# Kernel tuning notes

Hardware: AMD Instinct MI355X
Metric: run time of the kernel (lower is better)

## Reference

```python
import jax, jax.numpy as jnp
import numpy as np
import math

BS, S, D, H, DFF, L = 32, 512, 512, 8, 2048, 2
DK = D // H
K_INDEX = 5
NEG = -1e32


def _xavier(key, shape):
    fan_out, fan_in = shape[-2], shape[-1]
    lim = math.sqrt(6.0 / (fan_in + fan_out))
    return jax.random.uniform(key, shape, minval=-lim, maxval=lim, dtype=jnp.float32)


def _cosine_pe():
    pos = np.arange(S, dtype=np.float32)[:, None]
    div = np.exp(np.arange(0, D, 2, dtype=np.float32) * -(math.log(10000.0) / D))
    pe = np.zeros((S, D), dtype=np.float32)
    pe[:, 0::2] = np.sin(pos * div)
    pe[:, 1::2] = np.cos(pos * div)
    return jnp.asarray(pe)[None]  # [1,S,D]


def setup_inputs() -> dict:
    key = jax.random.key(0)
    ks = jax.random.split(key, 8)
    return {
        'q_embed_data': jax.random.normal(ks[0], (BS, S, D), jnp.float32),
        'qa_embed_data': jax.random.normal(ks[1], (BS, S, D), jnp.float32),
        'pe': _cosine_pe(),
        'Wk': _xavier(ks[2], (L, D, D)), 'bk': jnp.zeros((L, D)),
        'Wv': _xavier(ks[3], (L, D, D)), 'bv': jnp.zeros((L, D)),
        'Wo': _xavier(ks[4], (L, D, D)), 'bo': jnp.zeros((L, D)),
        'W1': _xavier(ks[5], (L, DFF, D)), 'b1': jnp.zeros((L, DFF)),
        'W2': _xavier(ks[6], (L, D, DFF)), 'b2': jnp.zeros((L, D)),
        'ln1w': jnp.ones((L, D)), 'ln1b': jnp.zeros((L, D)),
        'ln2w': jnp.ones((L, D)), 'ln2b': jnp.zeros((L, D)),
    }


def _ln(x, w, b):
    m = jnp.mean(x, axis=-1, keepdims=True)
    v = jnp.mean((x - m) ** 2, axis=-1, keepdims=True)
    return (x - m) / jnp.sqrt(v + 1e-5) * w + b


def _forward(q_embed_data, qa_embed_data, pe, Wk, bk, Wv, bv, Wo, bo,
             W1, b1, W2, b2, ln1w, ln1b, ln2w, ln2b):
    x = q_embed_data + pe[:, :S]
    y = qa_embed_data + pe[:, :S]
    # src_mask = (triu(ones, k=0) == 0): only strictly-lower positions allowed (row 0 fully masked)
    causal = jnp.tril(jnp.ones((S, S), bool), k=-1)
    attn_weights = None
    for l in range(L):
        # kq_same: q uses k_linear
        q = (x @ Wk[l].T + bk[l]).reshape(BS, S, H, DK).transpose(0, 2, 1, 3)
        k = q  # identical projection of identical input (key=query=x)
        v = (y @ Wv[l].T + bv[l]).reshape(BS, S, H, DK).transpose(0, 2, 1, 3)
        scores = jnp.einsum('bhqd,bhkd->bhqk', q, k) / math.sqrt(DK)
        scores = jnp.where(causal, scores, NEG)
        scores = jax.nn.softmax(scores, axis=-1)
        # sparseattn: for rows >= K_INDEX keep only entries >= k-th largest, re-softmax
        sb = scores[:, :, K_INDEX:, :]
        thr = jax.lax.top_k(sb, K_INDEX)[0][..., -1:]  # k-th largest per row
        sb = jnp.where(sb - thr >= 0, sb, NEG)
        scores = jnp.concatenate([scores[:, :, :K_INDEX, :], sb], axis=2)
        scores = jax.nn.softmax(scores, axis=-1)
        attn_weights = scores  # before_dropout_scores (before zero_pad)
        scores = scores.at[:, :, 0, :].set(0.0)  # zero_pad row 0
        out = jnp.einsum('bhqk,bhkd->bhqd', scores, v)
        out = out.transpose(0, 2, 1, 3).reshape(BS, S, D) @ Wo[l].T + bo[l]
        x = _ln(x + out, ln1w[l], ln1b[l])
        ff = jax.nn.relu(x @ W1[l].T + b1[l]) @ W2[l].T + b2[l]
        x = _ln(x + ff, ln2w[l], ln2b[l])
    return x, attn_weights


def reference(q_embed_data, qa_embed_data, pe, Wk, bk, Wv, bv, Wo, bo,
              W1, b1, W2, b2, ln1w, ln1b, ln2w, ln2b):
    return _forward(q_embed_data, qa_embed_data, pe, Wk, bk, Wv, bv, Wo, bo,
                    W1, b1, W2, b2, ln1w, ln1b, ln2w, ln2b)
```

## Files before the change

kernel.cpp:

```cpp
#include <hip/hip_runtime.h>
#include <hip/hip_bf16.h>
#include <math.h>

#define BSZ 32
#define SEQ 512
#define DIM 512
#define NH 8
#define DKH 64
#define DFFN 2048
#define NL 2
#define KIDX 5
#define NEGV -1e32f

typedef float f32x4 __attribute__((ext_vector_type(4)));
typedef short bf16x8 __attribute__((ext_vector_type(8)));
typedef unsigned short ushort_t;
typedef __attribute__((address_space(1))) void gvoid;
typedef __attribute__((address_space(3))) void lvoid;

__device__ __forceinline__ void gload_lds16(const void* g, void* l) {
    __builtin_amdgcn_global_load_lds((gvoid*)(uintptr_t)g, (lvoid*)l, 16, 0, 0);
}

__device__ __forceinline__ float wmaxf(float v) {
    #pragma unroll
    for (int m = 32; m > 0; m >>= 1) v = fmaxf(v, __shfl_xor(v, m));
    return v;
}
__device__ __forceinline__ float wsumf(float v) {
    #pragma unroll
    for (int m = 32; m > 0; m >>= 1) v += __shfl_xor(v, m);
    return v;
}
__device__ __forceinline__ int wsumi(int v) {
    #pragma unroll
    for (int m = 32; m > 0; m >>= 1) v += __shfl_xor(v, m);
    return v;
}

__device__ __forceinline__ unsigned int bf16_rne(float x) {
    unsigned int u = __float_as_uint(x);
    return (u + 0x7fffu + ((u >> 16) & 1u)) >> 16;
}
__device__ __forceinline__ void split3_8(const float* xs, unsigned int* hh,
                                         unsigned int* hm, unsigned int* hl) {
    #pragma unroll
    for (int e = 0; e < 8; e++) {
        float x = xs[e];
        unsigned int h0 = bf16_rne(x);
        float r1 = x - __uint_as_float(h0 << 16);
        unsigned int h1 = bf16_rne(r1);
        float r2 = r1 - __uint_as_float(h1 << 16);
        hh[e] = h0; hm[e] = h1; hl[e] = bf16_rne(r2);
    }
}
__device__ __forceinline__ uint4 pack8(const unsigned int* h) {
    return make_uint4(h[0] | (h[1] << 16), h[2] | (h[3] << 16),
                      h[4] | (h[5] << 16), h[6] | (h[7] << 16));
}

__device__ __forceinline__ f32x4 mfma_bf16(bf16x8 a, bf16x8 b, f32x4 c) {
    return __builtin_amdgcn_mfma_f32_16x16x32_bf16(a, b, c, 0, 0, 0);
}

__global__ void add_pe_new(const float* __restrict__ q, const float* __restrict__ qa,
                           const float* __restrict__ pe, float* __restrict__ x,
                           ushort_t* __restrict__ ypl, size_t yelems, int n8) {
    int i = blockIdx.x * 256 + threadIdx.x;
    if (i >= n8) return;
    size_t base = (size_t)i * 8;
    size_t pb = base & (size_t)(SEQ * DIM - 1);
    float4 a0 = *(const float4*)(q + base), a1 = *(const float4*)(q + base + 4);
    float4 b0 = *(const float4*)(qa + base), b1 = *(const float4*)(qa + base + 4);
    float4 p0 = *(const float4*)(pe + pb), p1 = *(const float4*)(pe + pb + 4);
    float4 x0 = make_float4(a0.x + p0.x, a0.y + p0.y, a0.z + p0.z, a0.w + p0.w);
    float4 x1 = make_float4(a1.x + p1.x, a1.y + p1.y, a1.z + p1.z, a1.w + p1.w);
    *(float4*)(x + base) = x0;
    *(float4*)(x + base + 4) = x1;
    float ys[8] = {b0.x + p0.x, b0.y + p0.y, b0.z + p0.z, b0.w + p0.w,
                   b1.x + p1.x, b1.y + p1.y, b1.z + p1.z, b1.w + p1.w};
    unsigned int hh[8], hm[8], hl[8];
    split3_8(ys, hh, hm, hl);
    *(uint4*)(ypl + base) = pack8(hh);
    *(uint4*)(ypl + yelems + base) = pack8(hm);
    *(uint4*)(ypl + 2 * yelems + base) = pack8(hl);
}

__global__ void split3w(const float* __restrict__ W, ushort_t* __restrict__ out,
                        size_t elems, int n8) {
    int i = blockIdx.x * 256 + threadIdx.x;
    if (i >= n8) return;
    size_t base = (size_t)i * 8;
    float4 a0 = *(const float4*)(W + base), a1 = *(const float4*)(W + base + 4);
    float xs[8] = {a0.x, a0.y, a0.z, a0.w, a1.x, a1.y, a1.z, a1.w};
    unsigned int hh[8], hm[8], hl[8];
    split3_8(xs, hh, hm, hl);
    *(uint4*)(out + base) = pack8(hh);
    *(uint4*)(out + elems + base) = pack8(hm);
    *(uint4*)(out + 2 * elems + base) = pack8(hl);
}

template <int RELU>
__global__ __launch_bounds__(256)
void gemm_bt(const float* __restrict__ A, const float* __restrict__ B,
             const float* __restrict__ bias, float* __restrict__ C,
             int M, int N, int K) {
    __shared__ float As[32][132];
    __shared__ float Bs[32][132];
    const int tid = threadIdx.x;
    const int tx = tid & 15, ty = tid >> 4;
    const int m0 = blockIdx.y * 128, n0 = blockIdx.x * 128;
    float acc[8][8] = {};
    for (int k0 = 0; k0 < K; k0 += 32) {
        #pragma unroll
        for (int s = tid; s < 1024; s += 256) {
            int r = (s & 15) | ((s >> 7) << 4);
            int c4 = (s >> 4) & 7;
            float4 va = *(const float4*)(A + (size_t)(m0 + r) * K + k0 + c4 * 4);
            As[c4 * 4 + 0][r] = va.x; As[c4 * 4 + 1][r] = va.y;
            As[c4 * 4 + 2][r] = va.z; As[c4 * 4 + 3][r] = va.w;
            float4 vb = *(const float4*)(B + (size_t)(n0 + r) * K + k0 + c4 * 4);
            Bs[c4 * 4 + 0][r] = vb.x; Bs[c4 * 4 + 1][r] = vb.y;
            Bs[c4 * 4 + 2][r] = vb.z; Bs[c4 * 4 + 3][r] = vb.w;
        }
        __syncthreads();
        #pragma unroll 8
        for (int kk = 0; kk < 32; kk++) {
            float a[8], b[8];
            *(float4*)&a[0] = *(const float4*)&As[kk][ty * 8];
            *(float4*)&a[4] = *(const float4*)&As[kk][ty * 8 + 4];
            *(float4*)&b[0] = *(const float4*)&Bs[kk][tx * 8];
            *(float4*)&b[4] = *(const float4*)&Bs[kk][tx * 8 + 4];
            #pragma unroll
            for (int i = 0; i < 8; i++)
                #pragma unroll
                for (int j = 0; j < 8; j++)
                    acc[i][j] = fmaf(a[i], b[j], acc[i][j]);
        }
        __syncthreads();
    }
    float bv[8];
    *(float4*)&bv[0] = *(const float4*)(bias + n0 + tx * 8);
    *(float4*)&bv[4] = *(const float4*)(bias + n0 + tx * 8 + 4);
    #pragma unroll
    for (int i = 0; i < 8; i++) {
        float out[8];
        #pragma unroll
        for (int j = 0; j < 8; j++) {
            float v = acc[i][j] + bv[j];
            if (RELU) v = fmaxf(v, 0.f);
            out[j] = v;
        }
        float* cp = C + (size_t)(m0 + ty * 8 + i) * N + n0 + tx * 8;
        *(float4*)cp = *(float4*)&out[0];
        *(float4*)(cp + 4) = *(float4*)&out[4];
    }
}

__global__ __launch_bounds__(256)
void scores128_kernel(const float* __restrict__ q, float* __restrict__ pbuf) {
    const int bh = blockIdx.y, b = bh >> 3, h = bh & 7;
    const int x = blockIdx.x;
    const int it = (x >= 6) ? 3 : (x >= 3) ? 2 : (x >= 1) ? 1 : 0;
    const int jt = x - it * (it + 1) / 2;
    const int m0 = it * 128, n0 = jt * 128;
    __shared__ float Qi[64][132];
    __shared__ float Qj[64][132];
    const float* qbase = q + (size_t)b * SEQ * DIM + h * DKH;
    const int tid = threadIdx.x;
    for (int s = tid; s < 2048; s += 256) {
        int row = (s & 15) | ((s >> 8) << 4);
        int c4 = (s >> 4) & 15;
        float4 vi = *(const float4*)(qbase + (size_t)(m0 + row) * DIM + c4 * 4);
        Qi[c4 * 4 + 0][row] = vi.x; Qi[c4 * 4 + 1][row] = vi.y;
        Qi[c4 * 4 + 2][row] = vi.z; Qi[c4 * 4 + 3][row] = vi.w;
        float4 vj = *(const float4*)(qbase + (size_t)(n0 + row) * DIM + c4 * 4);
        Qj[c4 * 4 + 0][row] = vj.x; Qj[c4 * 4 + 1][row] = vj.y;
        Qj[c4 * 4 + 2][row] = vj.z; Qj[c4 * 4 + 3][row] = vj.w;
    }
    __syncthreads();
    const int tx = tid & 15, ty = tid >> 4;
    float acc[8][8] = {};
    #pragma unroll 4
    for (int d = 0; d < 64; d++) {
        float a[8], bb[8];
        *(float4*)&a[0] = *(const float4*)&Qi[d][ty * 8];
        *(float4*)&a[4] = *(const float4*)&Qi[d][ty * 8 + 4];
        *(float4*)&bb[0] = *(const float4*)&Qj[d][tx * 8];
        *(float4*)&bb[4] = *(const float4*)&Qj[d][tx * 8 + 4];
        #pragma unroll
        for (int i = 0; i < 8; i++)
            #pragma unroll
            for (int j = 0; j < 8; j++)
                acc[i][j] = fmaf(a[i], bb[j], acc[i][j]);
    }
    float* prow = pbuf + ((size_t)bh * SEQ + m0) * SEQ + n0;
    #pragma unroll
    for (int i = 0; i < 8; i++) {
        int gi = m0 + ty * 8 + i;
        #pragma unroll
        for (int jq = 0; jq < 2; jq++) {
            float o[4];
            #pragma unroll
            for (int j = 0; j < 4; j++) {
                int gj = n0 + tx * 8 + jq * 4 + j;
                o[j] = (gj < gi) ? acc[i][jq * 4 + j] * 0.125f : NEGV;
            }
            *(float4*)(prow + (size_t)(ty * 8 + i) * SEQ + tx * 8 + jq * 4) = *(float4*)o;
        }
    }
}

template <int RELU, int OUTP, int NP>
__global__ __launch_bounds__(256) void gemm3p(
    const ushort_t* __restrict__ Apl, size_t Aelems, int lda,
    const ushort_t* __restrict__ Bpl, size_t Belems, int ldb,
    const float* __restrict__ bias,
    float* __restrict__ C, ushort_t* __restrict__ Cpl, size_t Celems,
    int ldc, int K) {
    constexpr int BB = NP * 512;
    __shared__ uint4 lds[2 * NP * 512];
    const int tid = threadIdx.x, lane = tid & 63, wid = tid >> 6;
    const int wm = wid >> 1, wn = wid & 1;
    const int m0 = blockIdx.y * 128, n0 = blockIdx.x * 128;
    const int lrow = lane & 15, lkof = (lane >> 4) * 8;
    f32x4 acc[4][4] = {};
    for (int k0 = 0; k0 < K; k0 += 32) {
        #pragma unroll
        for (int t = 0; t < 4 * NP; t++) {
            int cc = wid + t * 4;
            bool isB = cc >= 8 * NP;
            int c2 = isB ? (cc - 8 * NP) : cc;
            int p = c2 >> 3, fi = c2 & 7;
            const ushort_t* pb = isB ? (Bpl + (size_t)p * Belems) : (Apl + (size_t)p * Aelems);
            int ld = isB ? ldb : lda;
            int r0 = isB ? n0 : m0;
            const ushort_t* src = pb + (size_t)(r0 + fi * 16 + lrow) * ld + k0 + lkof;
            gload_lds16(src, &lds[(isB ? BB : 0) + p * 512 + fi * 64]);
        }
        __syncthreads();
        const bf16x8* ldsb = (const bf16x8*)lds;
        bf16x8 afr[4][NP];
        #pragma unroll
        for (int fm = 0; fm < 4; fm++)
            #pragma unroll
            for (int p = 0; p < NP; p++)
                afr[fm][p] = ldsb[p * 512 + (wm * 4 + fm) * 64 + lane];
        #pragma unroll
        for (int fn = 0; fn < 4; fn++) {
            bf16x8 b0 = ldsb[BB + 0 * 512 + (wn * 4 + fn) * 64 + lane];
            bf16x8 b1 = ldsb[BB + 1 * 512 + (wn * 4 + fn) * 64 + lane];
            bf16x8 b2;
            if constexpr (NP == 3) b2 = ldsb[BB + 2 * 512 + (wn * 4 + fn) * 64 + lane];
            #pragma unroll
            for (int fm = 0; fm < 4; fm++) {
                f32x4 t = acc[fm][fn];
                if constexpr (NP == 3) {
                    t = mfma_bf16(afr[fm][0], b0, t);
                    t = mfma_bf16(afr[fm][1], b0, t);
                    t = mfma_bf16(afr[fm][2], b0, t);
                    t = mfma_bf16(afr[fm][0], b1, t);
                    t = mfma_bf16(afr[fm][1], b1, t);
                    t = mfma_bf16(afr[fm][0], b2, t);
                } else {
                    t = mfma_bf16(afr[fm][0], b0, t);
                    t = mfma_bf16(afr[fm][1], b0, t);
                    t = mfma_bf16(afr[fm][0], b1, t);
                }
                acc[fm][fn] = t;
            }
        }
        __syncthreads();
    }
    #pragma unroll
    for (int fm = 0; fm < 4; fm++) {
        int row0 = m0 + (wm * 4 + fm) * 16 + (lane >> 4) * 4;
        #pragma unroll
        for (int fn = 0; fn < 4; fn++) {
            int col = n0 + (wn * 4 + fn) * 16 + (lane & 15);
            float bv = bias[col];
            f32x4 a = acc[fm][fn];
            #pragma unroll
            for (int r = 0; r < 4; r++) {
                int row = row0 + r;
                float val = a[r] + bv;
                if (RELU) val = fmaxf(val, 0.f);
                if constexpr (OUTP == 0) {
                    C[(size_t)row * ldc + col] = val;
                } else {
                    unsigned int h0 = bf16_rne(val);
                    float r1 = val - __uint_as_float(h0 << 16);
                    unsigned int h1 = bf16_rne(r1);
                    size_t o = (size_t)row * ldc + col;
                    Cpl[o] = (ushort_t)h0;
                    Cpl[Celems + o] = (ushort_t)h1;
                    if constexpr (NP == 3) {
                        float r2 = r1 - __uint_as_float(h1 << 16);
                        Cpl[2 * Celems + o] = (ushort_t)bf16_rne(r2);
                    }
                }
            }
        }
    }
}

template <int NP>
__global__ __launch_bounds__(256) void mm6av_pl(const float* __restrict__ pbuf,
                                                const float* __restrict__ vt,
                                                ushort_t* __restrict__ Opl, size_t Oelems) {
    constexpr int BBASE = NP * 512;
    __shared__ uint4 lds[NP * 512 + NP * 256];
    const int tid = threadIdx.x, lane = tid & 63, wid = tid >> 6;
    const int bh = blockIdx.y, b = bh >> 3, h = bh & 7, rb = blockIdx.x;
    const int m0 = rb * 128;
    const float* A = pbuf + (size_t)bh * SEQ * SEQ;
    const float* B = vt + (size_t)bh * DKH * SEQ;
    const int kmax = rb ? (rb + 1) * 128 : SEQ;

    f32x4 acc[2][4] = {};
    for (int k0 = 0; k0 < kmax; k0 += 32) {
        for (int c = tid; c < 12 * 64; c += 256) {
            int fi = c >> 6, lc = c & 63;
            const float* src = (fi < 8)
                ? A + (size_t)(m0 + fi * 16 + (lc & 15)) * SEQ + k0 + (lc >> 4) * 8
                : B + (size_t)((fi - 8) * 16 + (lc & 15)) * SEQ + k0 + (lc >> 4) * 8;
            float4 x0 = *(const float4*)src;
            float4 x1 = *(const float4*)(src + 4);
            float xs[8] = {x0.x, x0.y, x0.z, x0.w, x1.x, x1.y, x1.z, x1.w};
            unsigned int hh[8], hm[8], hl[8];
            split3_8(xs, hh, hm, hl);
            int base, fstride;
            if (fi < 8) { base = fi * 64 + lc; fstride = 512; }
            else { base = BBASE + (fi - 8) * 64 + lc; fstride = 256; }
            lds[base] = pack8(hh);
            lds[base + fstride] = pack8(hm);
            if (NP == 3) lds[base + 2 * fstride] = pack8(hl);
        }
        __syncthreads();
        const bf16x8* ldsb = (const bf16x8*)lds;
        bf16x8 afr[2][NP];
        #pragma unroll
        for (int fm = 0; fm < 2; fm++)
            #pragma unroll
            for (int p = 0; p < NP; p++)
                afr[fm][p] = ldsb[p * 512 + (wid * 2 + fm) * 64 + lane];
        #pragma unroll
        for (int fn = 0; fn < 4; fn++) {
            bf16x8 b0 = ldsb[BBASE + 0 * 256 + fn * 64 + lane];
            bf16x8 b1 = ldsb[BBASE + 1 * 256 + fn * 64 + lane];
            bf16x8 b2;
            if constexpr (NP == 3) b2 = ldsb[BBASE + 2 * 256 + fn * 64 + lane];
            #pragma unroll
            for (int fm = 0; fm < 2; fm++) {
                f32x4 t = acc[fm][fn];
                if constexpr (NP == 3) {
                    t = mfma_bf16(afr[fm][0], b0, t);
                    t = mfma_bf16(afr[fm][1], b0, t);
                    t = mfma_bf16(afr[fm][2], b0, t);
                    t = mfma_bf16(afr[fm][0], b1, t);
                    t = mfma_bf16(afr[fm][1], b1, t);
                    t = mfma_bf16(afr[fm][0], b2, t);
                } else {
                    t = mfma_bf16(afr[fm][0], b0, t);
                    t = mfma_bf16(afr[fm][1], b0, t);
                    t = mfma_bf16(afr[fm][0], b1, t);
                }
                acc[fm][fn] = t;
            }
        }
        __syncthreads();
    }
    #pragma unroll
    for (int fm = 0; fm < 2; fm++) {
        int row0 = m0 + (wid * 2 + fm) * 16 + (lane >> 4) * 4;
        #pragma unroll
        for (int fn = 0; fn < 4; fn++) {
            int col = fn * 16 + (lane & 15);
            f32x4 a = acc[fm][fn];
            #pragma unroll
            for (int r = 0; r < 4; r++) {
                int row = row0 + r;
                float val = (row == 0) ? 0.f : a[r];
                unsigned int h0 = bf16_rne(val);
                float r1 = val - __uint_as_float(h0 << 16);
                unsigned int h1 = bf16_rne(r1);
                size_t o = ((size_t)b * SEQ + row) * DIM + h * DKH + col;
                Opl[o] = (ushort_t)h0;
                Opl[Oelems + o] = (ushort_t)h1;
                if constexpr (NP == 3) {
                    float r2 = r1 - __uint_as_float(h1 << 16);
                    Opl[2 * Oelems + o] = (ushort_t)bf16_rne(r2);
                }
            }
        }
    }
}

__global__ __launch_bounds__(256) void transpose_v_kernel(const float* __restrict__ v,
                                                          float* __restrict__ vt) {
    const int bh = blockIdx.y, jt = blockIdx.x;
    const int b = bh >> 3, h = bh & 7;
    __shared__ float L[64][65];
    const int tid = threadIdx.x;
    for (int s = tid; s < 1024; s += 256) {
        int jj = s >> 4, d4 = s & 15;
        float4 x = *(const float4*)(v + ((size_t)(b * SEQ) + jt * 64 + jj) * DIM + h * DKH + d4 * 4);
        L[jj][d4 * 4 + 0] = x.x; L[jj][d4 * 4 + 1] = x.y;
        L[jj][d4 * 4 + 2] = x.z; L[jj][d4 * 4 + 3] = x.w;
    }
    __syncthreads();
    int d = tid >> 2, jq = tid & 3;
    float* dst = vt + ((size_t)bh * DKH + d) * SEQ + jt * 64 + jq * 16;
    #pragma unroll
    for (int c4 = 0; c4 < 4; c4++) {
        float4 o = make_float4(L[jq * 16 + c4 * 4 + 0][d], L[jq * 16 + c4 * 4 + 1][d],
                               L[jq * 16 + c4 * 4 + 2][d], L[jq * 16 + c4 * 4 + 3][d]);
        *(float4*)(dst + c4 * 4) = o;
    }
}

__global__ __launch_bounds__(256)
void softmax_topk_kernel(float* __restrict__ pbuf) {
    const int wid = threadIdx.x >> 6, lane = threadIdx.x & 63;
    const int i = blockIdx.x * 4 + wid;
    const size_t row = (size_t)blockIdx.y * SEQ + i;
    float* p = pbuf + row * SEQ;
    float v[8];
    {
        int j0 = lane * 4;
        if (j0 < i) {
            float4 x0 = *(const float4*)(p + j0);
            v[0] = (j0 + 0 < i) ? x0.x : NEGV;
            v[1] = (j0 + 1 < i) ? x0.y : NEGV;
            v[2] = (j0 + 2 < i) ? x0.z : NEGV;
            v[3] = (j0 + 3 < i) ? x0.w : NEGV;
        } else { v[0] = v[1] = v[2] = v[3] = NEGV; }
        int j1 = 256 + j0;
        if (j1 < i) {
            float4 x1 = *(const float4*)(p + j1);
            v[4] = (j1 + 0 < i) ? x1.x : NEGV;
            v[5] = (j1 + 1 < i) ? x1.y : NEGV;
            v[6] = (j1 + 2 < i) ? x1.z : NEGV;
            v[7] = (j1 + 3 < i) ? x1.w : NEGV;
        } else { v[4] = v[5] = v[6] = v[7] = NEGV; }
    }
    float lm = v[0];
    #pragma unroll
    for (int e = 1; e < 8; e++) lm = fmaxf(lm, v[e]);
    float m1 = wmaxf(lm);
    float ls = 0.f;
    #pragma unroll
    for (int e = 0; e < 8; e++) { v[e] = expf(v[e] - m1); ls += v[e]; }
    float Z = wsumf(ls);
    #pragma unroll
    for (int e = 0; e < 8; e++) v[e] = v[e] / Z;
    float thr = -INFINITY;
    if (i >= KIDX) {
        int remaining = KIDX;
        float cut = INFINITY;
        #pragma unroll 1
        for (int iter = 0; iter < KIDX; iter++) {
            float l2 = -INFINITY;
            #pragma unroll
            for (int e = 0; e < 8; e++) if (v[e] < cut) l2 = fmaxf(l2, v[e]);
            float m2 = wmaxf(l2);
            int lc = 0;
            #pragma unroll
            for (int e = 0; e < 8; e++) if (v[e] == m2) lc++;
            int c = wsumi(lc);
            if (c >= remaining) { thr = m2; break; }
            remaining -= c; cut = m2;
        }
    }
    float lpm = v[0];
    #pragma unroll
    for (int e = 1; e < 8; e++) lpm = fmaxf(lpm, v[e]);
    float pm = wmaxf(lpm);
    float t[8];
    float ls2 = 0.f;
    #pragma unroll
    for (int e = 0; e < 8; e++) {
        bool keep = (i >= KIDX) ? (v[e] >= thr) : true;
        t[e] = keep ? expf(v[e] - pm) : 0.f;
        ls2 += t[e];
    }
    float Z2 = wsumf(ls2);
    #pragma unroll
    for (int e = 0; e < 8; e++) t[e] = t[e] / Z2;
    *(float4*)(p + lane * 4) = make_float4(t[0], t[1], t[2], t[3]);
    *(float4*)(p + 256 + lane * 4) = make_float4(t[4], t[5], t[6], t[7]);
}

template <int EMIT>
__global__ __launch_bounds__(64)
void add_ln_kernel(const float* __restrict__ x, const float* __restrict__ t,
                   const float* __restrict__ w, const float* __restrict__ b,
                   float* __restrict__ dst, ushort_t* __restrict__ dpl, size_t delems) {
    const size_t row = blockIdx.x;
    const int lane = threadIdx.x;
    const float* xr = x + row * DIM;
    const float* tr = t + row * DIM;
    float v[8];
    {
        float4 a0 = *(const float4*)(xr + lane * 4);
        float4 t0 = *(const float4*)(tr + lane * 4);
        float4 a1 = *(const float4*)(xr + 256 + lane * 4);
        float4 t1 = *(const float4*)(tr + 256 + lane * 4);
        v[0] = a0.x + t0.x; v[1] = a0.y + t0.y; v[2] = a0.z + t0.z; v[3] = a0.w + t0.w;
        v[4] = a1.x + t1.x; v[5] = a1.y + t1.y; v[6] = a1.z + t1.z; v[7] = a1.w + t1.w;
    }
    float ls = 0.f;
    #pragma unroll
    for (int e = 0; e < 8; e++) ls += v[e];
    float mean = wsumf(ls) / (float)DIM;
    float ld = 0.f;
    #pragma unroll
    for (int e = 0; e < 8; e++) { float d = v[e] - mean; ld += d * d; }
    float var = wsumf(ld) / (float)DIM;
    float den = sqrtf(var + 1e-5f);
    float wv[8], bv[8];
    *(float4*)&wv[0] = *(const float4*)(w + lane * 4);
    *(float4*)&wv[4] = *(const float4*)(w + 256 + lane * 4);
    *(float4*)&bv[0] = *(const float4*)(b + lane * 4);
    *(float4*)&bv[4] = *(const float4*)(b + 256 + lane * 4);
    float o[8];
    #pragma unroll
    for (int e = 0; e < 8; e++) o[e] = (v[e] - mean) / den * wv[e] + bv[e];
    float* dr = dst + row * DIM;
    *(float4*)(dr + lane * 4) = make_float4(o[0], o[1], o[2], o[3]);
    *(float4*)(dr + 256 + lane * 4) = make_float4(o[4], o[5], o[6], o[7]);
    if constexpr (EMIT) {
        unsigned int hh[8], hm[8], hl[8];
        split3_8(o, hh, hm, hl);
        size_t base0 = row * DIM + lane * 4;
        size_t base1 = base0 + 256;
        #pragma unroll
        for (int p = 0; p < 3; p++) {
            const unsigned int* hp = (p == 0) ? hh : (p == 1) ? hm : hl;
            *(uint2*)(dpl + p * delems + base0) =
                make_uint2(hp[0] | (hp[1] << 16), hp[2] | (hp[3] << 16));
            *(uint2*)(dpl + p * delems + base1) =
                make_uint2(hp[4] | (hp[5] << 16), hp[6] | (hp[7] << 16));
        }
    }
}

extern "C" void kernel_launch(void* const* d_in, const int* in_sizes, int n_in,
                              void* d_out, int out_size, void* d_ws, size_t ws_size,
                              hipStream_t stream) {
    const float* q_embed = (const float*)d_in[0];
    const float* qa_embed = (const float*)d_in[1];
    const float* pe = (const float*)d_in[2];
    const float* Wk = (const float*)d_in[3];
    const float* bk = (const float*)d_in[4];
    const float* Wv = (const float*)d_in[5];
    const float* bv = (const float*)d_in[6];
    const float* Wo = (const float*)d_in[7];
    const float* bo = (const float*)d_in[8];
    const float* W1 = (const float*)d_in[9];
    const float* b1 = (const float*)d_in[10];
    const float* W2 = (const float*)d_in[11];
    const float* b2 = (const float*)d_in[12];
    const float* ln1w = (const float*)d_in[13];
    const float* ln1b = (const float*)d_in[14];
    const float* ln2w = (const float*)d_in[15];
    const float* ln2b = (const float*)d_in[16];

    float* outx = (float*)d_out;
    const size_t NE = (size_t)BSZ * SEQ * DIM;
    float* pbuf = outx + NE;
    float* ws = (float*)d_ws;
    const int M = BSZ * SEQ;

    float* xbuf = ws;
    float* qbuf = ws + NE;
    float* vbuf = ws + 2 * NE;
    ushort_t* y_pl = (ushort_t*)(ws + 3 * NE);
    ushort_t* x_pl = (ushort_t*)(ws + 4 * NE + NE / 2);
    ushort_t* w_pl = (ushort_t*)(ws + 6 * NE);
    float* vt = ws + 7 * NE;
    ushort_t* o_pl = (ushort_t*)(ws + 8 * NE);
    ushort_t* h1_pl = (ushort_t*)(ws + 7 * NE);

    const size_t WVE = (size_t)DIM * DIM;
    const size_t W1E = (size_t)DFFN * DIM;
    const size_t LW = 3 * (WVE + WVE + W1E + W1E);

    for (int l = 0; l < NL; l++) {
        ushort_t* base = w_pl + (size_t)l * LW;
        split3w<<<(int)(WVE / 8 + 255) / 256, 256, 0, stream>>>(
            Wv + (size_t)l * WVE, base, WVE, (int)(WVE / 8));
        split3w<<<(int)(WVE / 8 + 255) / 256, 256, 0, stream>>>(
            Wo + (size_t)l * WVE, base + 3 * WVE, WVE, (int)(WVE / 8));
        split3w<<<(int)(W1E / 8 + 255) / 256, 256, 0, stream>>>(
            W1 + (size_t)l * W1E, base + 6 * WVE, W1E, (int)(W1E / 8));
        split3w<<<(int)(W1E / 8 + 255) / 256, 256, 0, stream>>>(
            W2 + (size_t)l * W1E, base + 6 * WVE + 3 * W1E, W1E, (int)(W1E / 8));
    }

    add_pe_new<<<(int)(NE / 8 + 255) / 256, 256, 0, stream>>>(
        q_embed, qa_embed, pe, xbuf, y_pl, NE, (int)(NE / 8));

    for (int l = 0; l < NL; l++) {
        ushort_t* wb = w_pl + (size_t)l * LW;
        ushort_t* Wv_pl = wb;
        ushort_t* Wo_pl = wb + 3 * WVE;
        ushort_t* W1_pl = wb + 6 * WVE;
        ushort_t* W2_pl = wb + 6 * WVE + 3 * W1E;

        gemm_bt<0><<<dim3(DIM / 128, M / 128), 256, 0, stream>>>(
            xbuf, Wk + (size_t)l * WVE, bk + (size_t)l * DIM, qbuf, M, DIM, DIM);
        if (l == 0) {
            gemm3p<0, 0, 3><<<dim3(DIM / 128, M / 128), 256, 0, stream>>>(
                y_pl, NE, DIM, Wv_pl, WVE, DIM, bv + (size_t)l * DIM,
                vbuf, nullptr, 0, DIM, DIM);
        } else {
            gemm3p<0, 0, 2><<<dim3(DIM / 128, M / 128), 256, 0, stream>>>(
                y_pl, NE, DIM, Wv_pl, WVE, DIM, bv + (size_t)l * DIM,
                vbuf, nullptr, 0, DIM, DIM);
        }
        transpose_v_kernel<<<dim3(8, BSZ * NH), 256, 0, stream>>>(vbuf, vt);
        scores128_kernel<<<dim3(10, BSZ * NH), 256, 0, stream>>>(qbuf, pbuf);
        softmax_topk_kernel<<<dim3(SEQ / 4, BSZ * NH), 256, 0, stream>>>(pbuf);
        if (l == 0) {
            mm6av_pl<3><<<dim3(4, BSZ * NH), 256, 0, stream>>>(pbuf, vt, o_pl, NE);
            gemm3p<0, 0, 3><<<dim3(DIM / 128, M / 128), 256, 0, stream>>>(
                o_pl, NE, DIM, Wo_pl, WVE, DIM, bo + (size_t)l * DIM,
                qbuf, nullptr, 0, DIM, DIM);
        } else {
            mm6av_pl<2><<<dim3(4, BSZ * NH), 256, 0, stream>>>(pbuf, vt, o_pl, NE);
            gemm3p<0, 0, 2><<<dim3(DIM / 128, M / 128), 256, 0, stream>>>(
                o_pl, NE, DIM, Wo_pl, WVE, DIM, bo + (size_t)l * DIM,
                qbuf, nullptr, 0, DIM, DIM);
        }
        add_ln_kernel<1><<<M, 64, 0, stream>>>(
            xbuf, qbuf, ln1w + (size_t)l * DIM, ln1b + (size_t)l * DIM,
            xbuf, x_pl, NE);
        if (l == 0) {
            gemm3p<1, 1, 3><<<dim3(DFFN / 128, M / 128), 256, 0, stream>>>(
                x_pl, NE, DIM, W1_pl, W1E, DIM, b1 + (size_t)l * DFFN,
                nullptr, h1_pl, (size_t)M * DFFN, DFFN, DIM);
            gemm3p<0, 0, 3><<<dim3(DIM / 128, M / 128), 256, 0, stream>>>(
                h1_pl, (size_t)M * DFFN, DFFN, W2_pl, W1E, DFFN, b2 + (size_t)l * DIM,
                vbuf, nullptr, 0, DIM, DFFN);
        } else {
            gemm3p<1, 1, 2><<<dim3(DFFN / 128, M / 128), 256, 0, stream>>>(
                x_pl, NE, DIM, W1_pl, W1E, DIM, b1 + (size_t)l * DFFN,
                nullptr, h1_pl, (size_t)M * DFFN, DFFN, DIM);
            gemm3p<0, 0, 2><<<dim3(DIM / 128, M / 128), 256, 0, stream>>>(
                h1_pl, (size_t)M * DFFN, DFFN, W2_pl, W1E, DFFN, b2 + (size_t)l * DIM,
                vbuf, nullptr, 0, DIM, DFFN);
        }
        float* dst = (l == NL - 1) ? outx : xbuf;
        add_ln_kernel<0><<<M, 64, 0, stream>>>(
            xbuf, vbuf, ln2w + (size_t)l * DIM, ln2b + (size_t)l * DIM,
            dst, nullptr, 0);
    }
}
```

Measured before the change: 1.986 ms.

## Fuse score computation, top-k softmax and AV product into one attention kernel

Replaces three separate kernels (causal QK^T scores, sparse top-k softmax, split-bf16 AV matmul) with a single kernel launched per (row block, batch-head). Each block computes its lower-triangular score tiles sequentially, runs the two-pass softmax with top-k thresholding over its 128 rows, then performs the MFMA-based AV product, reusing one shared-memory buffer. The intent is to remove two kernel launches and keep the probability rows hot in cache between stages. In exchange the scores and softmax work lose parallelism: blocks are unevenly loaded along the causal diagonal and each wave now processes 32 rows serially.

New measurement: 2.448 ms. 1.23x slower.

```diff
diff --git a/kernel.cpp b/kernel.cpp
--- a/kernel.cpp
+++ b/kernel.cpp
@@ -157,56 +157,220 @@
     }
 }
 
-__global__ __launch_bounds__(256)
-void scores128_kernel(const float* __restrict__ q, float* __restrict__ pbuf) {
-    const int bh = blockIdx.y, b = bh >> 3, h = bh & 7;
-    const int x = blockIdx.x;
-    const int it = (x >= 6) ? 3 : (x >= 3) ? 2 : (x >= 1) ? 1 : 0;
-    const int jt = x - it * (it + 1) / 2;
-    const int m0 = it * 128, n0 = jt * 128;
-    __shared__ float Qi[64][132];
-    __shared__ float Qj[64][132];
+template <int NP>
+__global__ __launch_bounds__(256) void attn_fused(
+    const float* __restrict__ q, const float* __restrict__ vt,
+    float* __restrict__ pbuf, ushort_t* __restrict__ Opl, size_t Oelems) {
+    constexpr int BBASE = NP * 512;
+    __shared__ __align__(16) float smem[2 * 64 * 132];
+    float* Qi = smem;
+    float* Qj = smem + 64 * 132;
+    const int tid = threadIdx.x, lane = tid & 63, wid = tid >> 6;
+    const int bh = blockIdx.y, b = bh >> 3, h = bh & 7, rb = blockIdx.x;
+    const int m0 = rb * 128;
     const float* qbase = q + (size_t)b * SEQ * DIM + h * DKH;
-    const int tid = threadIdx.x;
+    float* prow_base = pbuf + (size_t)bh * SEQ * SEQ;
+
     for (int s = tid; s < 2048; s += 256) {
         int row = (s & 15) | ((s >> 8) << 4);
         int c4 = (s >> 4) & 15;
         float4 vi = *(const float4*)(qbase + (size_t)(m0 + row) * DIM + c4 * 4);
-        Qi[c4 * 4 + 0][row] = vi.x; Qi[c4 * 4 + 1][row] = vi.y;
-        Qi[c4 * 4 + 2][row] = vi.z; Qi[c4 * 4 + 3][row] = vi.w;
-        float4 vj = *(const float4*)(qbase + (size_t)(n0 + row) * DIM + c4 * 4);
-        Qj[c4 * 4 + 0][row] = vj.x; Qj[c4 * 4 + 1][row] = vj.y;
-        Qj[c4 * 4 + 2][row] = vj.z; Qj[c4 * 4 + 3][row] = vj.w;
+        Qi[(c4 * 4 + 0) * 132 + row] = vi.x; Qi[(c4 * 4 + 1) * 132 + row] = vi.y;
+        Qi[(c4 * 4 + 2) * 132 + row] = vi.z; Qi[(c4 * 4 + 3) * 132 + row] = vi.w;
+    }
+    const int tx = tid & 15, ty = tid >> 4;
+    for (int jt = 0; jt <= rb; jt++) {
+        const int n0 = jt * 128;
+        __syncthreads();
+        for (int s = tid; s < 2048; s += 256) {
+            int row = (s & 15) | ((s >> 8) << 4);
+            int c4 = (s >> 4) & 15;
+            float4 vj = *(const float4*)(qbase + (size_t)(n0 + row) * DIM + c4 * 4);
+            Qj[(c4 * 4 + 0) * 132 + row] = vj.x; Qj[(c4 * 4 + 1) * 132 + row] = vj.y;
+            Qj[(c4 * 4 + 2) * 132 + row] = vj.z; Qj[(c4 * 4 + 3) * 132 + row] = vj.w;
+        }
+        __syncthreads();
+        float acc[8][8] = {};
+        #pragma unroll 4
+        for (int d = 0; d < 64; d++) {
+            float a[8], bb[8];
+            *(float4*)&a[0] = *(const float4*)&Qi[d * 132 + ty * 8];
+            *(float4*)&a[4] = *(const float4*)&Qi[d * 132 + ty * 8 + 4];
+            *(float4*)&bb[0] = *(const float4*)&Qj[d * 132 + tx * 8];
+            *(float4*)&bb[4] = *(const float4*)&Qj[d * 132 + tx * 8 + 4];
+            #pragma unroll
+            for (int i = 0; i < 8; i++)
+                #pragma unroll
+                for (int j = 0; j < 8; j++)
+                    acc[i][j] = fmaf(a[i], bb[j], acc[i][j]);
+        }
+        float* prow = prow_base + (size_t)m0 * SEQ + n0;
+        #pragma unroll
+        for (int i = 0; i < 8; i++) {
+            int gi = m0 + ty * 8 + i;
+            #pragma unroll
+            for (int jq = 0; jq < 2; jq++) {
+                float o[4];
+                #pragma unroll
+                for (int j = 0; j < 4; j++) {
+                    int gj = n0 + tx * 8 + jq * 4 + j;
+                    o[j] = (gj < gi) ? acc[i][jq * 4 + j] * 0.125f : NEGV;
+                }
+                *(float4*)(prow + (size_t)(ty * 8 + i) * SEQ + tx * 8 + jq * 4) = *(float4*)o;
+            }
+        }
     }
     __syncthreads();
-    const int tx = tid & 15, ty = tid >> 4;
-    float acc[8][8] = {};
-    #pragma unroll 4
-    for (int d = 0; d < 64; d++) {
-        float a[8], bb[8];
-        *(float4*)&a[0] = *(const float4*)&Qi[d][ty * 8];
-        *(float4*)&a[4] = *(const float4*)&Qi[d][ty * 8 + 4];
-        *(float4*)&bb[0] = *(const float4*)&Qj[d][tx * 8];
-        *(float4*)&bb[4] = *(const float4*)&Qj[d][tx * 8 + 4];
-        #pragma unroll
-        for (int i = 0; i < 8; i++)
-            #pragma unroll
-            for (int j = 0; j < 8; j++)
-                acc[i][j] = fmaf(a[i], bb[j], acc[i][j]);
-    }
-    float* prow = pbuf + ((size_t)bh * SEQ + m0) * SEQ + n0;
-    #pragma unroll
-    for (int i = 0; i < 8; i++) {
-        int gi = m0 + ty * 8 + i;
-        #pragma unroll
-        for (int jq = 0; jq < 2; jq++) {
-            float o[4];
-            #pragma unroll
-            for (int j = 0; j < 4; j++) {
-                int gj = n0 + tx * 8 + jq * 4 + j;
-                o[j] = (gj < gi) ? acc[i][jq * 4 + j] * 0.125f : NEGV;
+
+    for (int t = 0; t < 32; t++) {
+        const int i = m0 + wid * 32 + t;
+        float* p = prow_base + (size_t)i * SEQ;
+        float v[8];
+        {
+            int j0 = lane * 4;
+            if (j0 < i) {
+                float4 x0 = *(const float4*)(p + j0);
+                v[0] = (j0 + 0 < i) ? x0.x : NEGV;
+                v[1] = (j0 + 1 < i) ? x0.y : NEGV;
+                v[2] = (j0 + 2 < i) ? x0.z : NEGV;
+                v[3] = (j0 + 3 < i) ? x0.w : NEGV;
+            } else { v[0] = v[1] = v[2] = v[3] = NEGV; }
+            int j1 = 256 + j0;
+            if (j1 < i) {
+                float4 x1 = *(const float4*)(p + j1);
+                v[4] = (j1 + 0 < i) ? x1.x : NEGV;
+                v[5] = (j1 + 1 < i) ? x1.y : NEGV;
+                v[6] = (j1 + 2 < i) ? x1.z : NEGV;
+                v[7] = (j1 + 3 < i) ? x1.w : NEGV;
+            } else { v[4] = v[5] = v[6] = v[7] = NEGV; }
+        }
+        float lm = v[0];
+        #pragma unroll
+        for (int e = 1; e < 8; e++) lm = fmaxf(lm, v[e]);
+        float m1 = wmaxf(lm);
+        float ls = 0.f;
+        #pragma unroll
+        for (int e = 0; e < 8; e++) { v[e] = expf(v[e] - m1); ls += v[e]; }
+        float Z = wsumf(ls);
+        #pragma unroll
+        for (int e = 0; e < 8; e++) v[e] = v[e] / Z;
+        float thr = -INFINITY;
+        if (i >= KIDX) {
+            int remaining = KIDX;
+            float cut = INFINITY;
+            #pragma unroll 1
+            for (int iter = 0; iter < KIDX; iter++) {
+                float l2 = -INFINITY;
+                #pragma unroll
+                for (int e = 0; e < 8; e++) if (v[e] < cut) l2 = fmaxf(l2, v[e]);
+                float m2 = wmaxf(l2);
+                int lc = 0;
+                #pragma unroll
+                for (int e = 0; e < 8; e++) if (v[e] == m2) lc++;
+                int c = wsumi(lc);
+                if (c >= remaining) { thr = m2; break; }
+                remaining -= c; cut = m2;
             }
-            *(float4*)(prow + (size_t)(ty * 8 + i) * SEQ + tx * 8 + jq * 4) = *(float4*)o;
+        }
+        float lpm = v[0];
+        #pragma unroll
+        for (int e = 1; e < 8; e++) lpm = fmaxf(lpm, v[e]);
+        float pm = wmaxf(lpm);
+        float tt[8];
+        float ls2 = 0.f;
+        #pragma unroll
+        for (int e = 0; e < 8; e++) {
+            bool keep = (i >= KIDX) ? (v[e] >= thr) : true;
+            tt[e] = keep ? expf(v[e] - pm) : 0.f;
+            ls2 += tt[e];
+        }
+        float Z2 = wsumf(ls2);
+        #pragma unroll
+        for (int e = 0; e < 8; e++) tt[e] = tt[e] / Z2;
+        *(float4*)(p + lane * 4) = make_float4(tt[0], tt[1], tt[2], tt[3]);
+        *(float4*)(p + 256 + lane * 4) = make_float4(tt[4], tt[5], tt[6], tt[7]);
+    }
+    __syncthreads();
+
+    uint4* lds = (uint4*)smem;
+    const float* A = prow_base;
+    const float* Bv = vt + (size_t)bh * DKH * SEQ;
+    const int kmax = rb ? (rb + 1) * 128 : SEQ;
+    f32x4 acc2[2][4] = {};
+    for (int k0 = 0; k0 < kmax; k0 += 32) {
+        for (int c = tid; c < 12 * 64; c += 256) {
+            int fi = c >> 6, lc = c & 63;
+            const float* src = (fi < 8)
+                ? A + (size_t)(m0 + fi * 16 + (lc & 15)) * SEQ + k0 + (lc >> 4) * 8
+                : Bv + (size_t)((fi - 8) * 16 + (lc & 15)) * SEQ + k0 + (lc >> 4) * 8;
+            float4 x0 = *(const float4*)src;
+            float4 x1 = *(const float4*)(src + 4);
+            float xs[8] = {x0.x, x0.y, x0.z, x0.w, x1.x, x1.y, x1.z, x1.w};
+            unsigned int hh[8], hm[8], hl[8];
+            split3_8(xs, hh, hm, hl);
+            int base, fstride;
+            if (fi < 8) { base = fi * 64 + lc; fstride = 512; }
+            else { base = BBASE + (fi - 8) * 64 + lc; fstride = 256; }
+            lds[base] = pack8(hh);
+            lds[base + fstride] = pack8(hm);
+            if (NP == 3) lds[base + 2 * fstride] = pack8(hl);
+        }
+        __syncthreads();
+        const bf16x8* ldsb = (const bf16x8*)lds;
+        bf16x8 afr[2][NP];
+        #pragma unroll
+        for (int fm = 0; fm < 2; fm++)
+            #pragma unroll
+            for (int p = 0; p < NP; p++)
+                afr[fm][p] = ldsb[p * 512 + (wid * 2 + fm) * 64 + lane];
+        #pragma unroll
+        for (int fn = 0; fn < 4; fn++) {
+            bf16x8 b0 = ldsb[BBASE + 0 * 256 + fn * 64 + lane];
+            bf16x8 b1 = ldsb[BBASE + 1 * 256 + fn * 64 + lane];
+            bf16x8 b2;
+            if constexpr (NP == 3) b2 = ldsb[BBASE + 2 * 256 + fn * 64 + lane];
+            #pragma unroll
+            for (int fm = 0; fm < 2; fm++) {
+                f32x4 t = acc2[fm][fn];
+                if constexpr (NP == 3) {
+                    t = mfma_bf16(afr[fm][0], b0, t);
+                    t = mfma_bf16(afr[fm][1], b0, t);
+                    t = mfma_bf16(afr[fm][2], b0, t);
+                    t = mfma_bf16(afr[fm][0], b1, t);
+                    t = mfma_bf16(afr[fm][1], b1, t);
+                    t = mfma_bf16(afr[fm][0], b2, t);
+                } else {
+                    t = mfma_bf16(afr[fm][0], b0, t);
+                    t = mfma_bf16(afr[fm][1], b0, t);
+                    t = mfma_bf16(afr[fm][0], b1, t);
+                }
+                acc2[fm][fn] = t;
+            }
+        }
+        __syncthreads();
+    }
+    #pragma unroll
+    for (int fm = 0; fm < 2; fm++) {
+        int row0 = m0 + (wid * 2 + fm) * 16 + (lane >> 4) * 4;
+        #pragma unroll
+        for (int fn = 0; fn < 4; fn++) {
+            int col = fn * 16 + (lane & 15);
+            f32x4 a = acc2[fm][fn];
+            #pragma unroll
+            for (int r = 0; r < 4; r++) {
+                int row = row0 + r;
+                float val = (row == 0) ? 0.f : a[r];
+                unsigned int h0 = bf16_rne(val);
+                float r1 = val - __uint_as_float(h0 << 16);
+                unsigned int h1 = bf16_rne(r1);
+                size_t o = ((size_t)b * SEQ + row) * DIM + h * DKH + col;
+                Opl[o] = (ushort_t)h0;
+                Opl[Oelems + o] = (ushort_t)h1;
+                if constexpr (NP == 3) {
+                    float r2 = r1 - __uint_as_float(h1 << 16);
+                    Opl[2 * Oelems + o] = (ushort_t)bf16_rne(r2);
+                }
+            }
         }
     }
 }
@@ -304,98 +468,6 @@
     }
 }
 
-template <int NP>
-__global__ __launch_bounds__(256) void mm6av_pl(const float* __restrict__ pbuf,
-                                                const float* __restrict__ vt,
-                                                ushort_t* __restrict__ Opl, size_t Oelems) {
-    constexpr int BBASE = NP * 512;
-    __shared__ uint4 lds[NP * 512 + NP * 256];
-    const int tid = threadIdx.x, lane = tid & 63, wid = tid >> 6;
-    const int bh = blockIdx.y, b = bh >> 3, h = bh & 7, rb = blockIdx.x;
-    const int m0 = rb * 128;
-    const float* A = pbuf + (size_t)bh * SEQ * SEQ;
-    const float* B = vt + (size_t)bh * DKH * SEQ;
-    const int kmax = rb ? (rb + 1) * 128 : SEQ;
-
-    f32x4 acc[2][4] = {};
-    for (int k0 = 0; k0 < kmax; k0 += 32) {
-        for (int c = tid; c < 12 * 64; c += 256) {
-            int fi = c >> 6, lc = c & 63;
-            const float* src = (fi < 8)
-                ? A + (size_t)(m0 + fi * 16 + (lc & 15)) * SEQ + k0 + (lc >> 4) * 8
-                : B + (size_t)((fi - 8) * 16 + (lc & 15)) * SEQ + k0 + (lc >> 4) * 8;
-            float4 x0 = *(const float4*)src;
-            float4 x1 = *(const float4*)(src + 4);
-            float xs[8] = {x0.x, x0.y, x0.z, x0.w, x1.x, x1.y, x1.z, x1.w};
-            unsigned int hh[8], hm[8], hl[8];
-            split3_8(xs, hh, hm, hl);
-            int base, fstride;
-            if (fi < 8) { base = fi * 64 + lc; fstride = 512; }
-            else { base = BBASE + (fi - 8) * 64 + lc; fstride = 256; }
-            lds[base] = pack8(hh);
-            lds[base + fstride] = pack8(hm);
-            if (NP == 3) lds[base + 2 * fstride] = pack8(hl);
-        }
-        __syncthreads();
-        const bf16x8* ldsb = (const bf16x8*)lds;
-        bf16x8 afr[2][NP];
-        #pragma unroll
-        for (int fm = 0; fm < 2; fm++)
-            #pragma unroll
-            for (int p = 0; p < NP; p++)
-                afr[fm][p] = ldsb[p * 512 + (wid * 2 + fm) * 64 + lane];
-        #pragma unroll
-        for (int fn = 0; fn < 4; fn++) {
-            bf16x8 b0 = ldsb[BBASE + 0 * 256 + fn * 64 + lane];
-            bf16x8 b1 = ldsb[BBASE + 1 * 256 + fn * 64 + lane];
-            bf16x8 b2;
-            if constexpr (NP == 3) b2 = ldsb[BBASE + 2 * 256 + fn * 64 + lane];
-            #pragma unroll
-            for (int fm = 0; fm < 2; fm++) {
-                f32x4 t = acc[fm][fn];
-                if constexpr (NP == 3) {
-                    t = mfma_bf16(afr[fm][0], b0, t);
-                    t = mfma_bf16(afr[fm][1], b0, t);
-                    t = mfma_bf16(afr[fm][2], b0, t);
-                    t = mfma_bf16(afr[fm][0], b1, t);
-                    t = mfma_bf16(afr[fm][1], b1, t);
-                    t = mfma_bf16(afr[fm][0], b2, t);
-                } else {
-                    t = mfma_bf16(afr[fm][0], b0, t);
-                    t = mfma_bf16(afr[fm][1], b0, t);
-                    t = mfma_bf16(afr[fm][0], b1, t);
-                }
-                acc[fm][fn] = t;
-            }
-        }
-        __syncthreads();
-    }
-    #pragma unroll
-    for (int fm = 0; fm < 2; fm++) {
-        int row0 = m0 + (wid * 2 + fm) * 16 + (lane >> 4) * 4;
-        #pragma unroll
-        for (int fn = 0; fn < 4; fn++) {
-            int col = fn * 16 + (lane & 15);
-            f32x4 a = acc[fm][fn];
-            #pragma unroll
-            for (int r = 0; r < 4; r++) {
-                int row = row0 + r;
-                float val = (row == 0) ? 0.f : a[r];
-                unsigned int h0 = bf16_rne(val);
-                float r1 = val - __uint_as_float(h0 << 16);
-                unsigned int h1 = bf16_rne(r1);
-                size_t o = ((size_t)b * SEQ + row) * DIM + h * DKH + col;
-                Opl[o] = (ushort_t)h0;
-                Opl[Oelems + o] = (ushort_t)h1;
-                if constexpr (NP == 3) {
-                    float r2 = r1 - __uint_as_float(h1 << 16);
-                    Opl[2 * Oelems + o] = (ushort_t)bf16_rne(r2);
-                }
-            }
-        }
-    }
-}
-
 __global__ __launch_bounds__(256) void transpose_v_kernel(const float* __restrict__ v,
                                                           float* __restrict__ vt) {
     const int bh = blockIdx.y, jt = blockIdx.x;
@@ -417,78 +489,6 @@
                                L[jq * 16 + c4 * 4 + 2][d], L[jq * 16 + c4 * 4 + 3][d]);
         *(float4*)(dst + c4 * 4) = o;
     }
-}
-
-__global__ __launch_bounds__(256)
-void softmax_topk_kernel(float* __restrict__ pbuf) {
-    const int wid = threadIdx.x >> 6, lane = threadIdx.x & 63;
-    const int i = blockIdx.x * 4 + wid;
-    const size_t row = (size_t)blockIdx.y * SEQ + i;
-    float* p = pbuf + row * SEQ;
-    float v[8];
-    {
-        int j0 = lane * 4;
-        if (j0 < i) {
-            float4 x0 = *(const float4*)(p + j0);
-            v[0] = (j0 + 0 < i) ? x0.x : NEGV;
-            v[1] = (j0 + 1 < i) ? x0.y : NEGV;
-            v[2] = (j0 + 2 < i) ? x0.z : NEGV;
-            v[3] = (j0 + 3 < i) ? x0.w : NEGV;
-        } else { v[0] = v[1] = v[2] = v[3] = NEGV; }
-        int j1 = 256 + j0;
-        if (j1 < i) {
-            float4 x1 = *(const float4*)(p + j1);
-            v[4] = (j1 + 0 < i) ? x1.x : NEGV;
-            v[5] = (j1 + 1 < i) ? x1.y : NEGV;
-            v[6] = (j1 + 2 < i) ? x1.z : NEGV;
-            v[7] = (j1 + 3 < i) ? x1.w : NEGV;
-        } else { v[4] = v[5] = v[6] = v[7] = NEGV; }
-    }
-    float lm = v[0];
-    #pragma unroll
-    for (int e = 1; e < 8; e++) lm = fmaxf(lm, v[e]);
-    float m1 = wmaxf(lm);
-    float ls = 0.f;
-    #pragma unroll
-    for (int e = 0; e < 8; e++) { v[e] = expf(v[e] - m1); ls += v[e]; }
-    float Z = wsumf(ls);
-    #pragma unroll
-    for (int e = 0; e < 8; e++) v[e] = v[e] / Z;
-    float thr = -INFINITY;
-    if (i >= KIDX) {
-        int remaining = KIDX;
-        float cut = INFINITY;
-        #pragma unroll 1
-        for (int iter = 0; iter < KIDX; iter++) {
-            float l2 = -INFINITY;
-            #pragma unroll
-            for (int e = 0; e < 8; e++) if (v[e] < cut) l2 = fmaxf(l2, v[e]);
-            float m2 = wmaxf(l2);
-            int lc = 0;
-            #pragma unroll
-            for (int e = 0; e < 8; e++) if (v[e] == m2) lc++;
-            int c = wsumi(lc);
-            if (c >= remaining) { thr = m2; break; }
-            remaining -= c; cut = m2;
-        }
-    }
-    float lpm = v[0];
-    #pragma unroll
-    for (int e = 1; e < 8; e++) lpm = fmaxf(lpm, v[e]);
-    float pm = wmaxf(lpm);
-    float t[8];
-    float ls2 = 0.f;
-    #pragma unroll
-    for (int e = 0; e < 8; e++) {
-        bool keep = (i >= KIDX) ? (v[e] >= thr) : true;
-        t[e] = keep ? expf(v[e] - pm) : 0.f;
-        ls2 += t[e];
-    }
-    float Z2 = wsumf(ls2);
-    #pragma unroll
-    for (int e = 0; e < 8; e++) t[e] = t[e] / Z2;
-    *(float4*)(p + lane * 4) = make_float4(t[0], t[1], t[2], t[3]);
-    *(float4*)(p + 256 + lane * 4) = make_float4(t[4], t[5], t[6], t[7]);
 }
 
 template <int EMIT>
@@ -620,15 +620,13 @@
                 vbuf, nullptr, 0, DIM, DIM);
         }
         transpose_v_kernel<<<dim3(8, BSZ * NH), 256, 0, stream>>>(vbuf, vt);
-        scores128_kernel<<<dim3(10, BSZ * NH), 256, 0, stream>>>(qbuf, pbuf);
-        softmax_topk_kernel<<<dim3(SEQ / 4, BSZ * NH), 256, 0, stream>>>(pbuf);
         if (l == 0) {
-            mm6av_pl<3><<<dim3(4, BSZ * NH), 256, 0, stream>>>(pbuf, vt, o_pl, NE);
+            attn_fused<3><<<dim3(4, BSZ * NH), 256, 0, stream>>>(qbuf, vt, pbuf, o_pl, NE);
             gemm3p<0, 0, 3><<<dim3(DIM / 128, M / 128), 256, 0, stream>>>(
                 o_pl, NE, DIM, Wo_pl, WVE, DIM, bo + (size_t)l * DIM,
                 qbuf, nullptr, 0, DIM, DIM);
         } else {
-            mm6av_pl<2><<<dim3(4, BSZ * NH), 256, 0, stream>>>(pbuf, vt, o_pl, NE);
+            attn_fused<2><<<dim3(4, BSZ * NH), 256, 0, stream>>>(qbuf, vt, pbuf, o_pl, NE);
             gemm3p<0, 0, 2><<<dim3(DIM / 128, M / 128), 256, 0, stream>>>(
                 o_pl, NE, DIM, Wo_pl, WVE, DIM, bo + (size_t)l * DIM,
                 qbuf, nullptr, 0, DIM, DIM);
```
